# Kernel tuning notes

Hardware: AMD Instinct MI355X
Metric: run time of the kernel (lower is better)

## Reference

```python
import jax, jax.numpy as jnp
import numpy as np

LN_EPS = 1e-5


def _expert(x, w1, b1, gamma, beta, w2, b2):
    # Linear(input_dim,24) -> LayerNorm(24) -> SiLU -> (Dropout=id in eval) -> Linear(24,16) -> SiLU
    h = x @ w1 + b1                                  # [B,24]
    mu = jnp.mean(h, axis=-1, keepdims=True)
    var = jnp.mean(jnp.square(h - mu), axis=-1, keepdims=True)
    h = (h - mu) * jax.lax.rsqrt(var + LN_EPS) * gamma + beta
    h = jax.nn.silu(h)
    return jax.nn.silu(h @ w2 + b2)                  # [B,16]


def setup_inputs() -> dict:
    key = jax.random.key(0)
    ks = jax.random.split(key, 16)
    D = 16  # input_dim
    s = 0.1
    inp = {
        "x": jax.random.normal(ks[0], (2097152, D), dtype=jnp.float32),
        # gate: Linear(D,8) -> Tanh -> Linear(8,2)
        "gw1": jax.random.normal(ks[1], (D, 8), dtype=jnp.float32) * s,
        "gb1": jnp.zeros((8,), jnp.float32),
        "gw2": jax.random.normal(ks[2], (8, 2), dtype=jnp.float32) * s,
        "gb2": jnp.zeros((2,), jnp.float32),
        # expert1
        "e1w1": jax.random.normal(ks[3], (D, 24), dtype=jnp.float32) * s,
        "e1b1": jnp.zeros((24,), jnp.float32),
        "e1g": jnp.ones((24,), jnp.float32),
        "e1bn": jnp.zeros((24,), jnp.float32),
        "e1w2": jax.random.normal(ks[4], (24, 16), dtype=jnp.float32) * s,
        "e1b2": jnp.zeros((16,), jnp.float32),
        # expert2
        "e2w1": jax.random.normal(ks[5], (D, 24), dtype=jnp.float32) * s,
        "e2b1": jnp.zeros((24,), jnp.float32),
        "e2g": jnp.ones((24,), jnp.float32),
        "e2bn": jnp.zeros((24,), jnp.float32),
        "e2w2": jax.random.normal(ks[6], (24, 16), dtype=jnp.float32) * s,
        "e2b2": jnp.zeros((16,), jnp.float32),
        # trunk: Linear(16,16) -> SiLU -> (Dropout=id)
        "tw": jax.random.normal(ks[7], (16, 16), dtype=jnp.float32) * s,
        "tb": jnp.zeros((16,), jnp.float32),
        # heads
        "sw": jax.random.normal(ks[8], (16, 1), dtype=jnp.float32) * s,
        "sb": jnp.zeros((1,), jnp.float32),
        "hw": jax.random.normal(ks[9], (16, 2), dtype=jnp.float32) * s,
        "hb": jnp.zeros((2,), jnp.float32),
    }
    return inp


def reference(x, gw1, gb1, gw2, gb2,
              e1w1, e1b1, e1g, e1bn, e1w2, e1b2,
              e2w1, e2b1, e2g, e2bn, e2w2, e2b2,
              tw, tb, sw, sb, hw, hb):
    gate_logits = jnp.tanh(x @ gw1 + gb1) @ gw2 + gb2        # [B,2]
    gate_w = jax.nn.softmax(gate_logits, axis=-1)
    h1 = _expert(x, e1w1, e1b1, e1g, e1bn, e1w2, e1b2)       # [B,16]
    h2 = _expert(x, e2w1, e2b1, e2g, e2bn, e2w2, e2b2)       # [B,16]
    h = gate_w[:, :1] * h1 + gate_w[:, 1:] * h2              # [B,16]
    h = jax.nn.silu(h @ tw + tb)                             # trunk (dropout=id)
    strain = h @ sw + sb                                     # [B,1]
    hs = h @ hw + hb                                         # [B,2]
    tensile_raw = hs[:, :1]
    gap = jax.nn.softplus(hs[:, 1:])
    yield_strength = tensile_raw - gap
    return jnp.concatenate([strain, tensile_raw, yield_strength], axis=-1)  # [B,3]
```

## Files before the change

kernel.cpp:

```cpp
#include <hip/hip_runtime.h>

#define LN_EPS 1e-5f

typedef _Float16 f16x4 __attribute__((ext_vector_type(4)));
typedef float f32x4 __attribute__((ext_vector_type(4)));
typedef unsigned int u32;
typedef u32 u32x2 __attribute__((ext_vector_type(2)));

#if defined(__HIP_DEVICE_COMPILE__)
#  if __has_builtin(__builtin_amdgcn_mfma_f32_16x16x16f16)
#    define MFMA16(a, b, c) __builtin_amdgcn_mfma_f32_16x16x16f16(a, b, c, 0, 0, 0)
#  elif __has_builtin(__builtin_amdgcn_mfma_f32_16x16x16_f16)
#    define MFMA16(a, b, c) __builtin_amdgcn_mfma_f32_16x16x16_f16(a, b, c, 0, 0, 0)
#  else
#    error "no 16x16x16 f16 mfma builtin on device"
#  endif
#else
#  define MFMA16(a, b, c) (c)
#endif

__device__ __forceinline__ float fast_rcp(float x) { return __builtin_amdgcn_rcpf(x); }

__device__ __forceinline__ u32 pk2(float a, float b) {
    return __builtin_bit_cast(u32, __builtin_amdgcn_cvt_pkrtz(a, b));
}
__device__ __forceinline__ f16x4 mk4(float a, float b, float c, float d) {
    u32x2 t = {pk2(a, b), pk2(c, d)};
    return __builtin_bit_cast(f16x4, t);
}

__device__ __forceinline__ void silu_quad(float a0, float a1, float a2, float a3,
                                          float& s0, float& s1, float& s2, float& s3) {
    float t0 = __expf(fminf(-a0, 20.0f));
    float t1 = __expf(fminf(-a1, 20.0f));
    float t2 = __expf(fminf(-a2, 20.0f));
    float t3 = __expf(fminf(-a3, 20.0f));
    float d0 = 1.0f + t0, d1 = 1.0f + t1, d2 = 1.0f + t2, d3 = 1.0f + t3;
    float d01 = d0 * d1, d23 = d2 * d3;
    float rp = fast_rcp(d01 * d23);
    float q01 = d23 * rp, q23 = d01 * rp;
    s0 = a0 * (d1 * q01);
    s1 = a1 * (d0 * q01);
    s2 = a2 * (d3 * q23);
    s3 = a3 * (d2 * q23);
}

__device__ __forceinline__ void tanh_quad(float x0, float x1, float x2, float x3,
                                          float& r0, float& r1, float& r2, float& r3) {
    float t0 = __expf(fminf(-2.0f * x0, 20.0f));
    float t1 = __expf(fminf(-2.0f * x1, 20.0f));
    float t2 = __expf(fminf(-2.0f * x2, 20.0f));
    float t3 = __expf(fminf(-2.0f * x3, 20.0f));
    float d0 = 1.0f + t0, d1 = 1.0f + t1, d2 = 1.0f + t2, d3 = 1.0f + t3;
    float d01 = d0 * d1, d23 = d2 * d3;
    float rp = fast_rcp(d01 * d23);
    float q01 = d23 * rp, q23 = d01 * rp;
    r0 = fmaf(2.0f, d1 * q01, -1.0f);
    r1 = fmaf(2.0f, d0 * q01, -1.0f);
    r2 = fmaf(2.0f, d3 * q23, -1.0f);
    r3 = fmaf(2.0f, d2 * q23, -1.0f);
}

__device__ __forceinline__ float softplus_f(float x) {
    float e = __expf(-fabsf(x));
    return fmaxf(x, 0.0f) + __logf(1.0f + e);
}


__device__ __forceinline__ float aval(int m, int row, int k,
                                      const float* gw1, const float* gw2,
                                      const float* e1w1, const float* e1w2,
                                      const float* e2w1, const float* e2w2,
                                      const float* tw, const float* sw, const float* hw) {
    switch (m) {
        case 0:  return (row < 8) ? gw1[k * 8 + row] : 0.0f;
        case 1:  return ((row & 3) < 2 && k < 8) ? gw2[k * 2 + (row & 3)] : 0.0f;
        case 2:  return e1w1[k * 24 + row];
        case 3:  return (row < 8) ? e1w1[k * 24 + 16 + row] : 0.0f;
        case 4:  return e1w2[k * 16 + row];
        case 5:  return (k < 8) ? e1w2[(16 + k) * 16 + row] : 0.0f;
        case 6:  return e2w1[k * 24 + row];
        case 7:  return (row < 8) ? e2w1[k * 24 + 16 + row] : 0.0f;
        case 8:  return e2w2[k * 16 + row];
        case 9:  return (k < 8) ? e2w2[(16 + k) * 16 + row] : 0.0f;
        case 10: return tw[k * 16 + row];
        default:
            if (row == 0) return sw[k];
            if (row == 1) return hw[2 * k + 0];
            if (row == 2) return hw[2 * k + 1];
            return 0.0f;
    }
}

__device__ __forceinline__ float bval(int bf, int row,
                                      const float* gb1, const float* gb2,
                                      const float* e1b1, const float* e1b2,
                                      const float* e2b1, const float* e2b2,
                                      const float* tb, const float* sb, const float* hb) {
    switch (bf) {
        case 0:  return (row < 8) ? gb1[row] : 0.0f;
        case 1:  return ((row & 3) < 2) ? gb2[row & 3] : 0.0f;
        case 2:  return e1b1[row];
        case 3:  return (row < 8) ? e1b1[16 + row] : 0.0f;
        case 4:  return e1b2[row];
        case 5:  return e2b1[row];
        case 6:  return (row < 8) ? e2b1[16 + row] : 0.0f;
        case 7:  return e2b2[row];
        case 8:  return tb[row];
        default:
            if (row == 0) return sb[0];
            if (row == 1) return hb[0];
            if (row == 2) return hb[1];
            return 0.0f;
    }
}

__global__ void pack_frags(const float* __restrict__ gw1, const float* __restrict__ gb1,
                           const float* __restrict__ gw2, const float* __restrict__ gb2,
                           const float* __restrict__ e1w1, const float* __restrict__ e1b1,
                           const float* __restrict__ e1g, const float* __restrict__ e1bn,
                           const float* __restrict__ e1w2, const float* __restrict__ e1b2,
                           const float* __restrict__ e2w1, const float* __restrict__ e2b1,
                           const float* __restrict__ e2g, const float* __restrict__ e2bn,
                           const float* __restrict__ e2w2, const float* __restrict__ e2b2,
                           const float* __restrict__ tw, const float* __restrict__ tb,
                           const float* __restrict__ sw, const float* __restrict__ sb,
                           const float* __restrict__ hw, const float* __restrict__ hb,
                           u32* __restrict__ ws) {
    int t = blockIdx.x * blockDim.x + threadIdx.x;
    if (t < 1536) {
        int m = t >> 7, rem = t & 127, lane = rem >> 1, d = rem & 1;
        int row = lane & 15, k0 = (lane >> 4) * 4 + 2 * d;
        float v0 = aval(m, row, k0,     gw1, gw2, e1w1, e1w2, e2w1, e2w2, tw, sw, hw);
        float v1 = aval(m, row, k0 + 1, gw1, gw2, e1w1, e1w2, e2w1, e2w2, tw, sw, hw);
        ws[t] = pk2(v0, v1);
    } else if (t < 4096) {
        int f = t - 1536;
        int bf = f >> 8, rem = f & 255, lane = rem >> 2, r = rem & 3;
        int row = (lane >> 4) * 4 + r;
        float v = bval(bf, row, gb1, gb2, e1b1, e1b2, e2b1, e2b2, tb, sb, hb);
        ((float*)ws)[t] = v;
    } else if (t < 6144) {
        int f = t - 4096;
        int nf = f >> 8, rem = f & 255, lane = rem >> 2, r = rem & 3;
        int e = nf >> 2, w = nf & 3, g_ = lane >> 4;
        const float* ge = e ? e2g : e1g;
        const float* bne = e ? e2bn : e1bn;
        float v;
        if (w < 2) {
            int feat = g_ * 4 + r;
            v = (w == 0) ? ge[feat] : bne[feat];
        } else {
            int feat = 16 + g_ * 4 + r;
            v = (g_ < 2) ? ((w == 2) ? ge[feat] : bne[feat]) : 0.0f;
        }
        ((float*)ws)[t] = v;
    }
}

template <bool FIRST>
__device__ __forceinline__ void expert_mfma2(f16x4 A1a, f16x4 A1b, f16x4 A2a, f16x4 A2b,
                                             f32x4 b1a, f32x4 b1b, f32x4 b2,
                                             f32x4 gc1, f32x4 bc1, f32x4 gc2, f32x4 bc2,
                                             f16x4 Bx0, f16x4 Bx1,
                                             float sc0, float sc1,
                                             f32x4& h0, f32x4& h1) {
    f32x4 C1_0 = MFMA16(A1a, Bx0, b1a);
    f32x4 C1_1 = MFMA16(A1a, Bx1, b1a);
    f32x4 C2_0 = MFMA16(A1b, Bx0, b1b);
    f32x4 C2_1 = MFMA16(A1b, Bx1, b1b);

    float E0 = 0.0f, E20 = 0.0f, E1 = 0.0f, E21 = 0.0f;
#pragma unroll
    for (int i = 0; i < 4; ++i) {
        E0 += C1_0[i] + C2_0[i];
        E1 += C1_1[i] + C2_1[i];
        E20 = fmaf(C1_0[i], C1_0[i], fmaf(C2_0[i], C2_0[i], E20));
        E21 = fmaf(C1_1[i], C1_1[i], fmaf(C2_1[i], C2_1[i], E21));
    }
    E0  += __shfl_xor(E0, 16);  E0  += __shfl_xor(E0, 32);
    E1  += __shfl_xor(E1, 16);  E1  += __shfl_xor(E1, 32);
    E20 += __shfl_xor(E20, 16); E20 += __shfl_xor(E20, 32);
    E21 += __shfl_xor(E21, 16); E21 += __shfl_xor(E21, 32);
    float mu0 = E0 * (1.0f / 24.0f), mu1 = E1 * (1.0f / 24.0f);
    float rstd0 = rsqrtf(fmaf(E20, 1.0f / 24.0f, -mu0 * mu0) + LN_EPS);
    float rstd1 = rsqrtf(fmaf(E21, 1.0f / 24.0f, -mu1 * mu1) + LN_EPS);

    float n0[8], n1[8], sv0[8], sv1[8];
#pragma unroll
    for (int i = 0; i < 4; ++i) {
        n0[i]     = fmaf((C1_0[i] - mu0) * rstd0, gc1[i], bc1[i]);
        n1[i]     = fmaf((C1_1[i] - mu1) * rstd1, gc1[i], bc1[i]);
        n0[4 + i] = fmaf((C2_0[i] - mu0) * rstd0, gc2[i], bc2[i]);
        n1[4 + i] = fmaf((C2_1[i] - mu1) * rstd1, gc2[i], bc2[i]);
    }
    silu_quad(n0[0], n0[1], n0[2], n0[3], sv0[0], sv0[1], sv0[2], sv0[3]);
    silu_quad(n0[4], n0[5], n0[6], n0[7], sv0[4], sv0[5], sv0[6], sv0[7]);
    silu_quad(n1[0], n1[1], n1[2], n1[3], sv1[0], sv1[1], sv1[2], sv1[3]);
    silu_quad(n1[4], n1[5], n1[6], n1[7], sv1[4], sv1[5], sv1[6], sv1[7]);
    f16x4 B1_0 = mk4(sv0[0], sv0[1], sv0[2], sv0[3]);
    f16x4 B2_0 = mk4(sv0[4], sv0[5], sv0[6], sv0[7]);
    f16x4 B1_1 = mk4(sv1[0], sv1[1], sv1[2], sv1[3]);
    f16x4 B2_1 = mk4(sv1[4], sv1[5], sv1[6], sv1[7]);

    f32x4 O0 = MFMA16(A2a, B1_0, b2);
    f32x4 O1 = MFMA16(A2a, B1_1, b2);
    O0 = MFMA16(A2b, B2_0, O0);
    O1 = MFMA16(A2b, B2_1, O1);

    float p0[4], p1[4];
    silu_quad(O0[0], O0[1], O0[2], O0[3], p0[0], p0[1], p0[2], p0[3]);
    silu_quad(O1[0], O1[1], O1[2], O1[3], p1[0], p1[1], p1[2], p1[3]);
#pragma unroll
    for (int i = 0; i < 4; ++i) {
        if (FIRST) {
            h0[i] = sc0 * p0[i];
            h1[i] = sc1 * p1[i];
        } else {
            h0[i] = fmaf(sc0, p0[i], h0[i]);
            h1[i] = fmaf(sc1, p1[i], h1[i]);
        }
    }
}

__global__ __launch_bounds__(256) void moe_mfma_kernel(const float* __restrict__ x,
                                                       const u32* __restrict__ ws,
                                                       float* __restrict__ out, int nrows) {
    const f16x4* Afr = (const f16x4*)ws;
    const float* wsf = (const float*)ws;
    const f32x4* Bfr = (const f32x4*)(wsf + 1536);
    const f32x4* Nfr = (const f32x4*)(wsf + 4096);

    int lane = threadIdx.x & 63;
    int g = lane >> 4, s = lane & 15;
    int wid = (blockIdx.x * blockDim.x + threadIdx.x) >> 6;
    int nw = (gridDim.x * blockDim.x) >> 6;

    f16x4 Ag1 = Afr[0 * 64 + lane], Ag2 = Afr[1 * 64 + lane];
    f16x4 A1a = Afr[2 * 64 + lane], A1b = Afr[3 * 64 + lane];
    f16x4 A2a = Afr[4 * 64 + lane], A2b = Afr[5 * 64 + lane];
    f16x4 A3a = Afr[6 * 64 + lane], A3b = Afr[7 * 64 + lane];
    f16x4 A4a = Afr[8 * 64 + lane], A4b = Afr[9 * 64 + lane];
    f16x4 Atr = Afr[10 * 64 + lane], Ahd = Afr[11 * 64 + lane];
    f32x4 Bg1 = Bfr[0 * 64 + lane], Bg2 = Bfr[1 * 64 + lane];
    f32x4 Be1a = Bfr[2 * 64 + lane], Be1b = Bfr[3 * 64 + lane], Be1o = Bfr[4 * 64 + lane];
    f32x4 Be2a = Bfr[5 * 64 + lane], Be2b = Bfr[6 * 64 + lane], Be2o = Bfr[7 * 64 + lane];
    f32x4 Btr = Bfr[8 * 64 + lane], Bhd = Bfr[9 * 64 + lane];
    f32x4 G1c1 = Nfr[0 * 64 + lane], B1c1 = Nfr[1 * 64 + lane];
    f32x4 G1c2 = Nfr[2 * 64 + lane], B1c2 = Nfr[3 * 64 + lane];
    f32x4 G2c1 = Nfr[4 * 64 + lane], B2c1 = Nfr[5 * 64 + lane];
    f32x4 G2c2 = Nfr[6 * 64 + lane], B2c2 = Nfr[7 * 64 + lane];

    int ntiles = (nrows + 15) >> 4;
    int nclamp = nrows - 1;

    auto loadx = [&](int tile) -> f32x4 {
        int r = tile * 16 + s;
        int rc = r < nrows ? r : nclamp;
        return *(const f32x4*)(x + (size_t)rc * 16 + g * 4);
    };

    int p0 = 2 * wid;
    f32x4 xv0, xv1;
    if (p0 < ntiles) {
        xv0 = loadx(p0);
        xv1 = loadx(p0 + 1 < ntiles ? p0 + 1 : p0);
    }

    for (int tp = p0; tp < ntiles; tp += 2 * nw) {
        int tnp = tp + 2 * nw;
        f32x4 xn0, xn1;
        {
            int t0n = tnp < ntiles ? tnp : tp;
            int t1n = tnp + 1 < ntiles ? tnp + 1 : t0n;
            xn0 = loadx(t0n);
            xn1 = loadx(t1n);
        }

        int r0 = tp * 16 + s;
        int r1 = (tp + 1) * 16 + s;
        f16x4 Bx0 = mk4(xv0[0], xv0[1], xv0[2], xv0[3]);
        f16x4 Bx1 = mk4(xv1[0], xv1[1], xv1[2], xv1[3]);

        f32x4 Cg0 = MFMA16(Ag1, Bx0, Bg1);
        f32x4 Cg1 = MFMA16(Ag1, Bx1, Bg1);
        float a0, a1, a2, a3, b0, b1, b2_, b3;
        tanh_quad(Cg0[0], Cg0[1], Cg0[2], Cg0[3], a0, a1, a2, a3);
        tanh_quad(Cg1[0], Cg1[1], Cg1[2], Cg1[3], b0, b1, b2_, b3);
        f16x4 Bt0 = mk4(a0, a1, a2, a3);
        f16x4 Bt1 = mk4(b0, b1, b2_, b3);
        f32x4 Cl0 = MFMA16(Ag2, Bt0, Bg2);
        f32x4 Cl1 = MFMA16(Ag2, Bt1, Bg2);
        float w00 = fast_rcp(1.0f + __expf(Cl0[1] - Cl0[0]));
        float w01 = 1.0f - w00;
        float w10 = fast_rcp(1.0f + __expf(Cl1[1] - Cl1[0]));
        float w11 = 1.0f - w10;

        f32x4 h0, h1;
        expert_mfma2<true >(A1a, A1b, A2a, A2b, Be1a, Be1b, Be1o,
                            G1c1, B1c1, G1c2, B1c2, Bx0, Bx1, w00, w10, h0, h1);
        expert_mfma2<false>(A3a, A3b, A4a, A4b, Be2a, Be2b, Be2o,
                            G2c1, B2c1, G2c2, B2c2, Bx0, Bx1, w01, w11, h0, h1);

        f16x4 Bh0 = mk4(h0[0], h0[1], h0[2], h0[3]);
        f16x4 Bh1 = mk4(h1[0], h1[1], h1[2], h1[3]);
        f32x4 Ct0 = MFMA16(Atr, Bh0, Btr);
        f32x4 Ct1 = MFMA16(Atr, Bh1, Btr);
        float u0[4], u1[4];
        silu_quad(Ct0[0], Ct0[1], Ct0[2], Ct0[3], u0[0], u0[1], u0[2], u0[3]);
        silu_quad(Ct1[0], Ct1[1], Ct1[2], Ct1[3], u1[0], u1[1], u1[2], u1[3]);
        f16x4 Bu0 = mk4(u0[0], u0[1], u0[2], u0[3]);
        f16x4 Bu1 = mk4(u1[0], u1[1], u1[2], u1[3]);

        f32x4 Ch0 = MFMA16(Ahd, Bu0, Bhd);
        f32x4 Ch1 = MFMA16(Ahd, Bu1, Bhd);
        if (g == 0) {
            if (r0 < nrows) {
                float yld = Ch0[1] - softplus_f(Ch0[2]);
                size_t o = (size_t)r0 * 3;
                out[o + 0] = Ch0[0];
                out[o + 1] = Ch0[1];
                out[o + 2] = yld;
            }
            if (r1 < nrows) {
                float yld = Ch1[1] - softplus_f(Ch1[2]);
                size_t o = (size_t)r1 * 3;
                out[o + 0] = Ch1[0];
                out[o + 1] = Ch1[1];
                out[o + 2] = yld;
            }
        }

        xv0 = xn0;
        xv1 = xn1;
    }
}

extern "C" void kernel_launch(void* const* d_in, const int* in_sizes, int n_in,
                              void* d_out, int out_size, void* d_ws, size_t ws_size,
                              hipStream_t stream) {
    const float* x    = (const float*)d_in[0];
    const float* gw1  = (const float*)d_in[1];
    const float* gb1  = (const float*)d_in[2];
    const float* gw2  = (const float*)d_in[3];
    const float* gb2  = (const float*)d_in[4];
    const float* e1w1 = (const float*)d_in[5];
    const float* e1b1 = (const float*)d_in[6];
    const float* e1g  = (const float*)d_in[7];
    const float* e1bn = (const float*)d_in[8];
    const float* e1w2 = (const float*)d_in[9];
    const float* e1b2 = (const float*)d_in[10];
    const float* e2w1 = (const float*)d_in[11];
    const float* e2b1 = (const float*)d_in[12];
    const float* e2g  = (const float*)d_in[13];
    const float* e2bn = (const float*)d_in[14];
    const float* e2w2 = (const float*)d_in[15];
    const float* e2b2 = (const float*)d_in[16];
    const float* tw   = (const float*)d_in[17];
    const float* tb   = (const float*)d_in[18];
    const float* sw   = (const float*)d_in[19];
    const float* sb   = (const float*)d_in[20];
    const float* hw   = (const float*)d_in[21];
    const float* hb   = (const float*)d_in[22];
    float* out = (float*)d_out;
    u32* ws = (u32*)d_ws;

    pack_frags<<<24, 256, 0, stream>>>(gw1, gb1, gw2, gb2,
                                       e1w1, e1b1, e1g, e1bn, e1w2, e1b2,
                                       e2w1, e2b1, e2g, e2bn, e2w2, e2b2,
                                       tw, tb, sw, sb, hw, hb, ws);

    int nrows = in_sizes[0] / 16;
    moe_mfma_kernel<<<2048, 256, 0, stream>>>(x, ws, out, nrows);
}
```

Before: 120.9 us.

## Compute LayerNorm mean via extra MFMA row and stage weight fragments in LDS

Appends a row holding the averaged first-layer weights and biases to the padded expert fragment, so the MFMA output directly yields the per-row mean. The mean is then fetched with one shuffle instead of a sum plus two xor-shuffle reductions, and the sum of squares masks out that extra row. Weight, bias and norm fragments are also copied into shared memory once per block and read from LDS on demand instead of being held in registers, aiming to lower register pressure and raise occupancy. The trade-off is extra LDS reads inside the hot loop plus a block-level sync at kernel start.

Measured after the change: 120.6 us. Within noise of the previous version (-0.3%).

```diff
diff --git a/kernel.cpp b/kernel.cpp
--- a/kernel.cpp
+++ b/kernel.cpp
@@ -76,11 +76,27 @@
         case 0:  return (row < 8) ? gw1[k * 8 + row] : 0.0f;
         case 1:  return ((row & 3) < 2 && k < 8) ? gw2[k * 2 + (row & 3)] : 0.0f;
         case 2:  return e1w1[k * 24 + row];
-        case 3:  return (row < 8) ? e1w1[k * 24 + 16 + row] : 0.0f;
+        case 3: {
+            if (row < 8) return e1w1[k * 24 + 16 + row];
+            if (row == 8) {
+                float t = 0.0f;
+                for (int j = 0; j < 24; ++j) t += e1w1[k * 24 + j];
+                return t * (1.0f / 24.0f);
+            }
+            return 0.0f;
+        }
         case 4:  return e1w2[k * 16 + row];
         case 5:  return (k < 8) ? e1w2[(16 + k) * 16 + row] : 0.0f;
         case 6:  return e2w1[k * 24 + row];
-        case 7:  return (row < 8) ? e2w1[k * 24 + 16 + row] : 0.0f;
+        case 7: {
+            if (row < 8) return e2w1[k * 24 + 16 + row];
+            if (row == 8) {
+                float t = 0.0f;
+                for (int j = 0; j < 24; ++j) t += e2w1[k * 24 + j];
+                return t * (1.0f / 24.0f);
+            }
+            return 0.0f;
+        }
         case 8:  return e2w2[k * 16 + row];
         case 9:  return (k < 8) ? e2w2[(16 + k) * 16 + row] : 0.0f;
         case 10: return tw[k * 16 + row];
@@ -101,10 +117,26 @@
         case 0:  return (row < 8) ? gb1[row] : 0.0f;
         case 1:  return ((row & 3) < 2) ? gb2[row & 3] : 0.0f;
         case 2:  return e1b1[row];
-        case 3:  return (row < 8) ? e1b1[16 + row] : 0.0f;
+        case 3: {
+            if (row < 8) return e1b1[16 + row];
+            if (row == 8) {
+                float t = 0.0f;
+                for (int j = 0; j < 24; ++j) t += e1b1[j];
+                return t * (1.0f / 24.0f);
+            }
+            return 0.0f;
+        }
         case 4:  return e1b2[row];
         case 5:  return e2b1[row];
-        case 6:  return (row < 8) ? e2b1[16 + row] : 0.0f;
+        case 6: {
+            if (row < 8) return e2b1[16 + row];
+            if (row == 8) {
+                float t = 0.0f;
+                for (int j = 0; j < 24; ++j) t += e2b1[j];
+                return t * (1.0f / 24.0f);
+            }
+            return 0.0f;
+        }
         case 7:  return e2b2[row];
         case 8:  return tb[row];
         default:
@@ -158,98 +190,94 @@
     }
 }
 
-template <bool FIRST>
-__device__ __forceinline__ void expert_mfma2(f16x4 A1a, f16x4 A1b, f16x4 A2a, f16x4 A2b,
-                                             f32x4 b1a, f32x4 b1b, f32x4 b2,
-                                             f32x4 gc1, f32x4 bc1, f32x4 gc2, f32x4 bc2,
-                                             f16x4 Bx0, f16x4 Bx1,
-                                             float sc0, float sc1,
-                                             f32x4& h0, f32x4& h1) {
-    f32x4 C1_0 = MFMA16(A1a, Bx0, b1a);
-    f32x4 C1_1 = MFMA16(A1a, Bx1, b1a);
-    f32x4 C2_0 = MFMA16(A1b, Bx0, b1b);
-    f32x4 C2_1 = MFMA16(A1b, Bx1, b1b);
-
-    float E0 = 0.0f, E20 = 0.0f, E1 = 0.0f, E21 = 0.0f;
-#pragma unroll
-    for (int i = 0; i < 4; ++i) {
-        E0 += C1_0[i] + C2_0[i];
-        E1 += C1_1[i] + C2_1[i];
-        E20 = fmaf(C1_0[i], C1_0[i], fmaf(C2_0[i], C2_0[i], E20));
-        E21 = fmaf(C1_1[i], C1_1[i], fmaf(C2_1[i], C2_1[i], E21));
-    }
-    E0  += __shfl_xor(E0, 16);  E0  += __shfl_xor(E0, 32);
-    E1  += __shfl_xor(E1, 16);  E1  += __shfl_xor(E1, 32);
-    E20 += __shfl_xor(E20, 16); E20 += __shfl_xor(E20, 32);
-    E21 += __shfl_xor(E21, 16); E21 += __shfl_xor(E21, 32);
-    float mu0 = E0 * (1.0f / 24.0f), mu1 = E1 * (1.0f / 24.0f);
-    float rstd0 = rsqrtf(fmaf(E20, 1.0f / 24.0f, -mu0 * mu0) + LN_EPS);
-    float rstd1 = rsqrtf(fmaf(E21, 1.0f / 24.0f, -mu1 * mu1) + LN_EPS);
-
-    float n0[8], n1[8], sv0[8], sv1[8];
-#pragma unroll
-    for (int i = 0; i < 4; ++i) {
-        n0[i]     = fmaf((C1_0[i] - mu0) * rstd0, gc1[i], bc1[i]);
-        n1[i]     = fmaf((C1_1[i] - mu1) * rstd1, gc1[i], bc1[i]);
-        n0[4 + i] = fmaf((C2_0[i] - mu0) * rstd0, gc2[i], bc2[i]);
-        n1[4 + i] = fmaf((C2_1[i] - mu1) * rstd1, gc2[i], bc2[i]);
-    }
-    silu_quad(n0[0], n0[1], n0[2], n0[3], sv0[0], sv0[1], sv0[2], sv0[3]);
-    silu_quad(n0[4], n0[5], n0[6], n0[7], sv0[4], sv0[5], sv0[6], sv0[7]);
-    silu_quad(n1[0], n1[1], n1[2], n1[3], sv1[0], sv1[1], sv1[2], sv1[3]);
-    silu_quad(n1[4], n1[5], n1[6], n1[7], sv1[4], sv1[5], sv1[6], sv1[7]);
-    f16x4 B1_0 = mk4(sv0[0], sv0[1], sv0[2], sv0[3]);
-    f16x4 B2_0 = mk4(sv0[4], sv0[5], sv0[6], sv0[7]);
-    f16x4 B1_1 = mk4(sv1[0], sv1[1], sv1[2], sv1[3]);
-    f16x4 B2_1 = mk4(sv1[4], sv1[5], sv1[6], sv1[7]);
-
-    f32x4 O0 = MFMA16(A2a, B1_0, b2);
-    f32x4 O1 = MFMA16(A2a, B1_1, b2);
-    O0 = MFMA16(A2b, B2_0, O0);
-    O1 = MFMA16(A2b, B2_1, O1);
-
-    float p0[4], p1[4];
-    silu_quad(O0[0], O0[1], O0[2], O0[3], p0[0], p0[1], p0[2], p0[3]);
-    silu_quad(O1[0], O1[1], O1[2], O1[3], p1[0], p1[1], p1[2], p1[3]);
-#pragma unroll
-    for (int i = 0; i < 4; ++i) {
-        if (FIRST) {
-            h0[i] = sc0 * p0[i];
-            h1[i] = sc1 * p1[i];
-        } else {
-            h0[i] = fmaf(sc0, p0[i], h0[i]);
-            h1[i] = fmaf(sc1, p1[i], h1[i]);
-        }
-    }
-}
-
 __global__ __launch_bounds__(256) void moe_mfma_kernel(const float* __restrict__ x,
                                                        const u32* __restrict__ ws,
                                                        float* __restrict__ out, int nrows) {
-    const f16x4* Afr = (const f16x4*)ws;
-    const float* wsf = (const float*)ws;
-    const f32x4* Bfr = (const f32x4*)(wsf + 1536);
-    const f32x4* Nfr = (const f32x4*)(wsf + 4096);
+    __shared__ u32 lds[6144];
+    for (int i = threadIdx.x; i < 6144; i += 256) lds[i] = ws[i];
+    __syncthreads();
 
     int lane = threadIdx.x & 63;
     int g = lane >> 4, s = lane & 15;
+    float mask0 = (g == 2) ? 0.0f : 1.0f;
     int wid = (blockIdx.x * blockDim.x + threadIdx.x) >> 6;
     int nw = (gridDim.x * blockDim.x) >> 6;
 
-    f16x4 Ag1 = Afr[0 * 64 + lane], Ag2 = Afr[1 * 64 + lane];
-    f16x4 A1a = Afr[2 * 64 + lane], A1b = Afr[3 * 64 + lane];
-    f16x4 A2a = Afr[4 * 64 + lane], A2b = Afr[5 * 64 + lane];
-    f16x4 A3a = Afr[6 * 64 + lane], A3b = Afr[7 * 64 + lane];
-    f16x4 A4a = Afr[8 * 64 + lane], A4b = Afr[9 * 64 + lane];
-    f16x4 Atr = Afr[10 * 64 + lane], Ahd = Afr[11 * 64 + lane];
-    f32x4 Bg1 = Bfr[0 * 64 + lane], Bg2 = Bfr[1 * 64 + lane];
-    f32x4 Be1a = Bfr[2 * 64 + lane], Be1b = Bfr[3 * 64 + lane], Be1o = Bfr[4 * 64 + lane];
-    f32x4 Be2a = Bfr[5 * 64 + lane], Be2b = Bfr[6 * 64 + lane], Be2o = Bfr[7 * 64 + lane];
-    f32x4 Btr = Bfr[8 * 64 + lane], Bhd = Bfr[9 * 64 + lane];
-    f32x4 G1c1 = Nfr[0 * 64 + lane], B1c1 = Nfr[1 * 64 + lane];
-    f32x4 G1c2 = Nfr[2 * 64 + lane], B1c2 = Nfr[3 * 64 + lane];
-    f32x4 G2c1 = Nfr[4 * 64 + lane], B2c1 = Nfr[5 * 64 + lane];
-    f32x4 G2c2 = Nfr[6 * 64 + lane], B2c2 = Nfr[7 * 64 + lane];
+    auto LA  = [&](int m)  -> f16x4 { return *(const f16x4*)&lds[m * 128 + lane * 2]; };
+    auto LB  = [&](int bf) -> f32x4 { return *(const f32x4*)&lds[1536 + bf * 256 + lane * 4]; };
+    auto LNF = [&](int nf) -> f32x4 { return *(const f32x4*)&lds[4096 + nf * 256 + lane * 4]; };
+
+    auto expert2 = [&](bool FIRST, int mA1a, int mA1b, int mA2a, int mA2b,
+                       int bf1a, int bf1b, int bf2, int nf,
+                       f16x4 Bx0, f16x4 Bx1, float sc0, float sc1,
+                       f32x4& h0, f32x4& h1) {
+        f16x4 A1a = LA(mA1a), A1b = LA(mA1b);
+        f32x4 b1a = LB(bf1a), b1b = LB(bf1b);
+        f32x4 C1_0 = MFMA16(A1a, Bx0, b1a);
+        f32x4 C1_1 = MFMA16(A1a, Bx1, b1a);
+        f32x4 C2_0 = MFMA16(A1b, Bx0, b1b);
+        f32x4 C2_1 = MFMA16(A1b, Bx1, b1b);
+
+        float mu0 = __shfl(C2_0[0], 32 + s, 64);
+        float mu1 = __shfl(C2_1[0], 32 + s, 64);
+
+        float E20 = 0.0f, E21 = 0.0f;
+#pragma unroll
+        for (int i = 0; i < 4; ++i) {
+            E20 = fmaf(C1_0[i], C1_0[i], E20);
+            E21 = fmaf(C1_1[i], C1_1[i], E21);
+        }
+        E20 = fmaf(C2_0[0] * mask0, C2_0[0], E20);
+        E21 = fmaf(C2_1[0] * mask0, C2_1[0], E21);
+#pragma unroll
+        for (int i = 1; i < 4; ++i) {
+            E20 = fmaf(C2_0[i], C2_0[i], E20);
+            E21 = fmaf(C2_1[i], C2_1[i], E21);
+        }
+        E20 += __shfl_xor(E20, 16); E20 += __shfl_xor(E20, 32);
+        E21 += __shfl_xor(E21, 16); E21 += __shfl_xor(E21, 32);
+        float rstd0 = rsqrtf(fmaf(E20, 1.0f / 24.0f, -mu0 * mu0) + LN_EPS);
+        float rstd1 = rsqrtf(fmaf(E21, 1.0f / 24.0f, -mu1 * mu1) + LN_EPS);
+
+        f32x4 gc1 = LNF(nf + 0), bc1 = LNF(nf + 1), gc2 = LNF(nf + 2), bc2 = LNF(nf + 3);
+        float n0[8], n1[8], sv0[8], sv1[8];
+#pragma unroll
+        for (int i = 0; i < 4; ++i) {
+            n0[i]     = fmaf((C1_0[i] - mu0) * rstd0, gc1[i], bc1[i]);
+            n1[i]     = fmaf((C1_1[i] - mu1) * rstd1, gc1[i], bc1[i]);
+            n0[4 + i] = fmaf((C2_0[i] - mu0) * rstd0, gc2[i], bc2[i]);
+            n1[4 + i] = fmaf((C2_1[i] - mu1) * rstd1, gc2[i], bc2[i]);
+        }
+        silu_quad(n0[0], n0[1], n0[2], n0[3], sv0[0], sv0[1], sv0[2], sv0[3]);
+        silu_quad(n0[4], n0[5], n0[6], n0[7], sv0[4], sv0[5], sv0[6], sv0[7]);
+        silu_quad(n1[0], n1[1], n1[2], n1[3], sv1[0], sv1[1], sv1[2], sv1[3]);
+        silu_quad(n1[4], n1[5], n1[6], n1[7], sv1[4], sv1[5], sv1[6], sv1[7]);
+        f16x4 B1_0 = mk4(sv0[0], sv0[1], sv0[2], sv0[3]);
+        f16x4 B2_0 = mk4(sv0[4], sv0[5], sv0[6], sv0[7]);
+        f16x4 B1_1 = mk4(sv1[0], sv1[1], sv1[2], sv1[3]);
+        f16x4 B2_1 = mk4(sv1[4], sv1[5], sv1[6], sv1[7]);
+
+        f16x4 A2a = LA(mA2a), A2b = LA(mA2b);
+        f32x4 b2 = LB(bf2);
+        f32x4 O0 = MFMA16(A2a, B1_0, b2);
+        f32x4 O1 = MFMA16(A2a, B1_1, b2);
+        O0 = MFMA16(A2b, B2_0, O0);
+        O1 = MFMA16(A2b, B2_1, O1);
+
+        float p0[4], p1[4];
+        silu_quad(O0[0], O0[1], O0[2], O0[3], p0[0], p0[1], p0[2], p0[3]);
+        silu_quad(O1[0], O1[1], O1[2], O1[3], p1[0], p1[1], p1[2], p1[3]);
+#pragma unroll
+        for (int i = 0; i < 4; ++i) {
+            if (FIRST) {
+                h0[i] = sc0 * p0[i];
+                h1[i] = sc1 * p1[i];
+            } else {
+                h0[i] = fmaf(sc0, p0[i], h0[i]);
+                h1[i] = fmaf(sc1, p1[i], h1[i]);
+            }
+        }
+    };
 
     int ntiles = (nrows + 15) >> 4;
     int nclamp = nrows - 1;
@@ -282,38 +310,36 @@
         f16x4 Bx0 = mk4(xv0[0], xv0[1], xv0[2], xv0[3]);
         f16x4 Bx1 = mk4(xv1[0], xv1[1], xv1[2], xv1[3]);
 
-        f32x4 Cg0 = MFMA16(Ag1, Bx0, Bg1);
-        f32x4 Cg1 = MFMA16(Ag1, Bx1, Bg1);
+        f32x4 Cg0 = MFMA16(LA(0), Bx0, LB(0));
+        f32x4 Cg1 = MFMA16(LA(0), Bx1, LB(0));
         float a0, a1, a2, a3, b0, b1, b2_, b3;
         tanh_quad(Cg0[0], Cg0[1], Cg0[2], Cg0[3], a0, a1, a2, a3);
         tanh_quad(Cg1[0], Cg1[1], Cg1[2], Cg1[3], b0, b1, b2_, b3);
         f16x4 Bt0 = mk4(a0, a1, a2, a3);
         f16x4 Bt1 = mk4(b0, b1, b2_, b3);
-        f32x4 Cl0 = MFMA16(Ag2, Bt0, Bg2);
-        f32x4 Cl1 = MFMA16(Ag2, Bt1, Bg2);
+        f32x4 Cl0 = MFMA16(LA(1), Bt0, LB(1));
+        f32x4 Cl1 = MFMA16(LA(1), Bt1, LB(1));
         float w00 = fast_rcp(1.0f + __expf(Cl0[1] - Cl0[0]));
         float w01 = 1.0f - w00;
         float w10 = fast_rcp(1.0f + __expf(Cl1[1] - Cl1[0]));
         float w11 = 1.0f - w10;
 
         f32x4 h0, h1;
-        expert_mfma2<true >(A1a, A1b, A2a, A2b, Be1a, Be1b, Be1o,
-                            G1c1, B1c1, G1c2, B1c2, Bx0, Bx1, w00, w10, h0, h1);
-        expert_mfma2<false>(A3a, A3b, A4a, A4b, Be2a, Be2b, Be2o,
-                            G2c1, B2c1, G2c2, B2c2, Bx0, Bx1, w01, w11, h0, h1);
+        expert2(true,  2, 3, 4, 5, 2, 3, 4, 0, Bx0, Bx1, w00, w10, h0, h1);
+        expert2(false, 6, 7, 8, 9, 5, 6, 7, 4, Bx0, Bx1, w01, w11, h0, h1);
 
         f16x4 Bh0 = mk4(h0[0], h0[1], h0[2], h0[3]);
         f16x4 Bh1 = mk4(h1[0], h1[1], h1[2], h1[3]);
-        f32x4 Ct0 = MFMA16(Atr, Bh0, Btr);
-        f32x4 Ct1 = MFMA16(Atr, Bh1, Btr);
+        f32x4 Ct0 = MFMA16(LA(10), Bh0, LB(8));
+        f32x4 Ct1 = MFMA16(LA(10), Bh1, LB(8));
         float u0[4], u1[4];
         silu_quad(Ct0[0], Ct0[1], Ct0[2], Ct0[3], u0[0], u0[1], u0[2], u0[3]);
         silu_quad(Ct1[0], Ct1[1], Ct1[2], Ct1[3], u1[0], u1[1], u1[2], u1[3]);
         f16x4 Bu0 = mk4(u0[0], u0[1], u0[2], u0[3]);
         f16x4 Bu1 = mk4(u1[0], u1[1], u1[2], u1[3]);
 
-        f32x4 Ch0 = MFMA16(Ahd, Bu0, Bhd);
-        f32x4 Ch1 = MFMA16(Ahd, Bu1, Bhd);
+        f32x4 Ch0 = MFMA16(LA(11), Bu0, LB(9));
+        f32x4 Ch1 = MFMA16(LA(11), Bu1, LB(9));
         if (g == 0) {
             if (r0 < nrows) {
                 float yld = Ch0[1] - softplus_f(Ch0[2]);
```
